# Optimization experiments

Hardware: AMD Instinct MI355X
Metric: run time of the kernel (lower is better)

## Reference

```python
import jax, jax.numpy as jnp
import numpy as np

NUM_GRAPHS = 2048


def gcn_conv(x, W, b, edge, N):
    # PyG GCNConv: x' = D^{-1/2} (A + I) D^{-1/2} (x W) + b
    src, dst = edge[0], edge[1]
    loop = jnp.arange(N, dtype=src.dtype)
    src = jnp.concatenate([src, loop])
    dst = jnp.concatenate([dst, loop])
    h = x @ W  # [N, out]
    deg = jax.ops.segment_sum(jnp.ones(dst.shape, x.dtype), dst, num_segments=N)
    dinv = jnp.where(deg > 0, jax.lax.rsqrt(deg), 0.0)
    norm = dinv[src] * dinv[dst]  # [E+N]
    out = jax.ops.segment_sum(h[src] * norm[:, None], dst, num_segments=N)
    return out + b


def pool_max_mean(x, batch, G):
    mx = jax.ops.segment_max(x, batch, num_segments=G)
    mx = jnp.where(jnp.isfinite(mx), mx, 0.0)  # guard empty segments
    s = jax.ops.segment_sum(x, batch, num_segments=G)
    cnt = jax.ops.segment_sum(jnp.ones((x.shape[0],), x.dtype), batch, num_segments=G)
    mean = s / jnp.maximum(cnt, 1.0)[:, None]
    return mx, mean


def setup_inputs() -> dict:
    key = jax.random.key(0)
    ks = jax.random.split(key, 20)
    F, CE, SE, DD = 64, 64, 32, 128
    Nc, Ec, Ns, Es = 100000, 1250000, 100000, 1250000

    def glorot(k, shape):
        fan_in, fan_out = shape[0], shape[1]
        lim = np.sqrt(6.0 / (fan_in + fan_out)).astype(np.float32)
        return jax.random.uniform(k, shape, jnp.float32, -lim, lim)

    inp = {
        "c": jax.random.normal(ks[0], (Nc, F), jnp.float32),
        "c_edge": jax.random.randint(ks[1], (2, Ec), 0, Nc),
        "c_batch": jnp.sort(jax.random.randint(ks[2], (Nc,), 0, NUM_GRAPHS)),
        "s": jax.random.normal(ks[3], (Ns, F), jnp.float32),
        "s_edge": jax.random.randint(ks[4], (2, Es), 0, Ns),
        "s_batch": jnp.sort(jax.random.randint(ks[5], (Ns,), 0, NUM_GRAPHS)),
        "Wc0": glorot(ks[6], (F, CE)), "bc0": jnp.zeros((CE,), jnp.float32),
        "Wc1": glorot(ks[7], (CE, CE)), "bc1": jnp.zeros((CE,), jnp.float32),
        "Wc2": glorot(ks[8], (CE, CE)), "bc2": jnp.zeros((CE,), jnp.float32),
        "Ws0": glorot(ks[9], (F, SE)), "bs0": jnp.zeros((SE,), jnp.float32),
        "Ws1": glorot(ks[10], (SE, SE)), "bs1": jnp.zeros((SE,), jnp.float32),
        "Ws2": glorot(ks[11], (SE, SE)), "bs2": jnp.zeros((SE,), jnp.float32),
        "Wd": glorot(ks[12], ((CE + SE) * 2, DD)), "bd": jnp.zeros((DD,), jnp.float32),
        "Wo": glorot(ks[13], (DD, 1)), "bo": jnp.zeros((1,), jnp.float32),
    }
    return inp


def reference(c, c_edge, c_batch, s, s_edge, s_batch,
              Wc0, bc0, Wc1, bc1, Wc2, bc2,
              Ws0, bs0, Ws1, bs1, Ws2, bs2,
              Wd, bd, Wo, bo):
    Nc, Ns = c.shape[0], s.shape[0]
    cro = jax.nn.relu(gcn_conv(c, Wc0, bc0, c_edge, Nc))
    cro = jax.nn.relu(gcn_conv(cro, Wc1, bc1, c_edge, Nc))
    cro = jax.nn.relu(gcn_conv(cro, Wc2, bc2, c_edge, Nc))
    solv = jax.nn.relu(gcn_conv(s, Ws0, bs0, s_edge, Ns))
    solv = jax.nn.relu(gcn_conv(solv, Ws1, bs1, s_edge, Ns))
    solv = jax.nn.relu(gcn_conv(solv, Ws2, bs2, s_edge, Ns))
    c_mx, c_mean = pool_max_mean(cro, c_batch, NUM_GRAPHS)
    s_mx, s_mean = pool_max_mean(solv, s_batch, NUM_GRAPHS)
    embed = jnp.concatenate([c_mx, c_mean, s_mx, s_mean], axis=1)  # [G, 192]
    dense = jax.nn.relu(embed @ Wd + bd)
    out = dense @ Wo + bo  # [G, 1]
    return out, embed
```

## Files before the change

kernel.cpp:

```cpp
#include <hip/hip_runtime.h>
#include <hip/hip_fp16.h>
#include <math.h>


static inline int cdiv(int a, int b) { return (a + b - 1) / b; }

#define BUCKET_CAP 8192
#define P1_CHUNK   4096

typedef _Float16 v8h __attribute__((ext_vector_type(8)));
typedef float    v4f __attribute__((ext_vector_type(4)));

__global__ void zero_int(int* __restrict__ p, int n) {
    int i = blockIdx.x * blockDim.x + threadIdx.x;
    if (i < n) p[i] = 0;
}

__global__ __launch_bounds__(256) void p1_partition(const int* __restrict__ c_edge, int Ec,
                                                    const int* __restrict__ s_edge, int Es,
                                                    int Nc_pad, int Etot, int nbuck,
                                                    int* __restrict__ bucket_fill,
                                                    unsigned* __restrict__ pk) {
    __shared__ unsigned       wbuf[P1_CHUNK];
    __shared__ unsigned short bbuf[P1_CHUNK];
    __shared__ int            hist[512];
    int e0 = blockIdx.x * P1_CHUNK;
    int n  = Etot - e0;
    if (n > P1_CHUNK) n = P1_CHUNK;
    for (int i = threadIdx.x; i < nbuck; i += 256) hist[i] = 0;
    __syncthreads();
    for (int i = threadIdx.x; i < n; i += 256) {
        int e = e0 + i, src, g;
        if (e < Ec) { src = c_edge[e]; g = c_edge[Ec + e]; }
        else        { int e2 = e - Ec; src = s_edge[e2]; g = Nc_pad + s_edge[Es + e2]; }
        int b   = g >> 9;
        wbuf[i] = ((unsigned)(g & 511) << 17) | (unsigned)src;
        bbuf[i] = (unsigned short)b;
        atomicAdd(&hist[b], 1);
    }
    __syncthreads();
    for (int i = threadIdx.x; i < nbuck; i += 256) {
        int h = hist[i];
        hist[i] = h ? atomicAdd(&bucket_fill[i], h) : 0;
    }
    __syncthreads();
    for (int i = threadIdx.x; i < n; i += 256) {
        int b    = bbuf[i];
        int slot = atomicAdd(&hist[b], 1);
        if (slot < BUCKET_CAP) pk[(size_t)b * BUCKET_CAP + slot] = wbuf[i];
    }
}

__global__ __launch_bounds__(512) void p2_scanbuckets(const int* __restrict__ fill, int nbuck,
                                                      int* __restrict__ basearr,
                                                      int* __restrict__ off_all, int Ntot_pad, int Etot) {
    __shared__ int sh[512];
    int v = (threadIdx.x < nbuck) ? fill[threadIdx.x] : 0;
    sh[threadIdx.x] = v;
    __syncthreads();
    for (int ofs = 1; ofs < 512; ofs <<= 1) {
        int t = (threadIdx.x >= ofs) ? sh[threadIdx.x - ofs] : 0;
        __syncthreads();
        sh[threadIdx.x] += t;
        __syncthreads();
    }
    if (threadIdx.x < nbuck) basearr[threadIdx.x] = sh[threadIdx.x] - v;
    if (threadIdx.x == 0) off_all[Ntot_pad] = Etot;
}

__global__ __launch_bounds__(512) void p3_build(const unsigned* __restrict__ pk,
                                                const int* __restrict__ fillarr,
                                                const int* __restrict__ basearr,
                                                int* __restrict__ off_all,
                                                float* __restrict__ dinv,
                                                int* __restrict__ csr) {
    __shared__ int sh[512];
    int b    = blockIdx.x;
    int fill = fillarr[b];
    if (fill > BUCKET_CAP) fill = BUCKET_CAP;
    int base = basearr[b];
    const unsigned* reg = pk + (size_t)b * BUCKET_CAP;
    sh[threadIdx.x] = 0;
    __syncthreads();
    for (int i = threadIdx.x; i < fill; i += 512) atomicAdd(&sh[reg[i] >> 17], 1);
    __syncthreads();
    int cnt = sh[threadIdx.x];
    for (int ofs = 1; ofs < 512; ofs <<= 1) {
        int t = (threadIdx.x >= ofs) ? sh[threadIdx.x - ofs] : 0;
        __syncthreads();
        sh[threadIdx.x] += t;
        __syncthreads();
    }
    int excl = sh[threadIdx.x] - cnt;
    int node = b * 512 + threadIdx.x;
    off_all[node] = base + excl;
    dinv[node]    = rsqrtf((float)(cnt + 1));
    __syncthreads();
    sh[threadIdx.x] = excl;
    __syncthreads();
    for (int i = threadIdx.x; i < fill; i += 512) {
        unsigned w    = reg[i];
        int      slot = atomicAdd(&sh[w >> 17], 1);
        csr[base + slot] = (int)(w & 0x1FFFFu);
    }
}

template <int K, int M, typename TIN>
__device__ void gemm_mfma(int bid, const TIN* __restrict__ X, const float* __restrict__ W,
                          const float* __restrict__ dinv, __half* __restrict__ H, int N,
                          char* smem_) {
    constexpr int RB = 64;
    constexpr int KP = K + 8;
    constexpr int NT = M / 16;
    constexpr int KS = K / 32;
    _Float16* Xh = (_Float16*)smem_;
    _Float16* Wz = Xh + RB * KP;
    const int t    = threadIdx.x;
    const int row0 = bid * RB;

    constexpr int WENT = NT * KS * 64;
    for (int idx = t; idx < WENT; idx += 256) {
        int lane = idx & 63, rest = idx >> 6;
        int ks = rest % KS, ntl = rest / KS;
        int kbase = ks * 32 + (lane >> 4) * 8;
        int col   = ntl * 16 + (lane & 15);
        union { float4 f4; _Float16 h[8]; } u;
#pragma unroll
        for (int j = 0; j < 8; ++j) u.h[j] = (_Float16)W[(kbase + j) * M + col];
        *(float4*)(Wz + idx * 8) = u.f4;
    }
    if constexpr (sizeof(TIN) == 4) {
        constexpr int NI = RB * K / 4;
        for (int idx = t; idx < NI; idx += 256) {
            int row = idx / (K / 4), k4 = idx % (K / 4);
            int gr = row0 + row;
            float4 v = make_float4(0.f, 0.f, 0.f, 0.f);
            if (gr < N) v = *(const float4*)((const float*)X + (size_t)gr * K + k4 * 4);
            union { float2 f2; _Float16 h[4]; } u;
            u.h[0] = (_Float16)v.x; u.h[1] = (_Float16)v.y;
            u.h[2] = (_Float16)v.z; u.h[3] = (_Float16)v.w;
            *(float2*)(Xh + row * KP + k4 * 4) = u.f2;
        }
    } else {
        constexpr int NI = RB * K / 8;
        for (int idx = t; idx < NI; idx += 256) {
            int row = idx / (K / 8), k8 = idx % (K / 8);
            int gr = row0 + row;
            float4 v = make_float4(0.f, 0.f, 0.f, 0.f);
            if (gr < N) v = *(const float4*)((const __half*)X + (size_t)gr * K + k8 * 8);
            *(float4*)(Xh + row * KP + k8 * 8) = v;
        }
    }
    __syncthreads();

    const int wave = t >> 6, lane = t & 63;
    const int quad = lane >> 4, nl = lane & 15;
    const int rowA = wave * 16 + nl;

    v4f acc[NT];
#pragma unroll
    for (int i = 0; i < NT; ++i) acc[i] = (v4f){0.f, 0.f, 0.f, 0.f};

#pragma unroll
    for (int ks = 0; ks < KS; ++ks) {
        v8h a = *(const v8h*)(Xh + rowA * KP + ks * 32 + quad * 8);
#pragma unroll
        for (int ntl = 0; ntl < NT; ++ntl) {
            v8h b = *(const v8h*)(Wz + ((ntl * KS + ks) * 64 + lane) * 8);
            acc[ntl] = __builtin_amdgcn_mfma_f32_16x16x32_f16(a, b, acc[ntl], 0, 0, 0);
        }
    }

#pragma unroll
    for (int r = 0; r < 4; ++r) {
        int gr = row0 + wave * 16 + quad * 4 + r;
        if (gr < N) {
            float dv = dinv[gr];
#pragma unroll
            for (int ntl = 0; ntl < NT; ++ntl)
                H[(size_t)gr * M + ntl * 16 + nl] = __float2half(acc[ntl][r] * dv);
        }
    }
}

__device__ __forceinline__ float4 load4h(const float2* __restrict__ base, size_t idx) {
    float2 r = base[idx];
    union { float2 f2; __half2 h2[2]; } u;
    u.f2 = r;
    float2 a = __half22float2(u.h2[0]);
    float2 b = __half22float2(u.h2[1]);
    return make_float4(a.x, a.y, b.x, b.y);
}

template <int M>
__device__ void agg_body(int bid, const __half* __restrict__ H,
                         const int* __restrict__ off_g,
                         const int* __restrict__ csr,
                         const float* __restrict__ dinv_g,
                         const float* __restrict__ b,
                         __half* __restrict__ out, int Nloc) {
    constexpr int L   = M / 4;
    constexpr int NPW = 64 / L;
    int lane = threadIdx.x & 63;
    int wave = threadIdx.x >> 6;
    int fq   = lane & (L - 1);
    int sub  = lane / L;
    int node = (bid * 4 + wave) * NPW + sub;
    if (node >= Nloc) return;
    const float2* H4 = (const float2*)H;
    int j0 = off_g[node], j1 = off_g[node + 1];
    float4 acc = load4h(H4, (size_t)node * L + fq);
    int j = j0;
    for (; j + 8 <= j1; j += 8) {
        int s0 = csr[j],     s1 = csr[j + 1], s2 = csr[j + 2], s3 = csr[j + 3];
        int s4 = csr[j + 4], s5 = csr[j + 5], s6 = csr[j + 6], s7 = csr[j + 7];
        float4 a0 = load4h(H4, (size_t)s0 * L + fq);
        float4 a1 = load4h(H4, (size_t)s1 * L + fq);
        float4 a2 = load4h(H4, (size_t)s2 * L + fq);
        float4 a3 = load4h(H4, (size_t)s3 * L + fq);
        float4 a4 = load4h(H4, (size_t)s4 * L + fq);
        float4 a5 = load4h(H4, (size_t)s5 * L + fq);
        float4 a6 = load4h(H4, (size_t)s6 * L + fq);
        float4 a7 = load4h(H4, (size_t)s7 * L + fq);
        acc.x += (a0.x + a1.x + a2.x + a3.x) + (a4.x + a5.x + a6.x + a7.x);
        acc.y += (a0.y + a1.y + a2.y + a3.y) + (a4.y + a5.y + a6.y + a7.y);
        acc.z += (a0.z + a1.z + a2.z + a3.z) + (a4.z + a5.z + a6.z + a7.z);
        acc.w += (a0.w + a1.w + a2.w + a3.w) + (a4.w + a5.w + a6.w + a7.w);
    }
    for (; j + 4 <= j1; j += 4) {
        int s0 = csr[j], s1 = csr[j + 1], s2 = csr[j + 2], s3 = csr[j + 3];
        float4 a0 = load4h(H4, (size_t)s0 * L + fq);
        float4 a1 = load4h(H4, (size_t)s1 * L + fq);
        float4 a2 = load4h(H4, (size_t)s2 * L + fq);
        float4 a3 = load4h(H4, (size_t)s3 * L + fq);
        acc.x += a0.x + a1.x + a2.x + a3.x;
        acc.y += a0.y + a1.y + a2.y + a3.y;
        acc.z += a0.z + a1.z + a2.z + a3.z;
        acc.w += a0.w + a1.w + a2.w + a3.w;
    }
    for (; j < j1; ++j) {
        float4 a = load4h(H4, (size_t)csr[j] * L + fq);
        acc.x += a.x; acc.y += a.y; acc.z += a.z; acc.w += a.w;
    }
    float  dv = dinv_g[node];
    float4 bb = ((const float4*)b)[fq];
    float  vx = dv * acc.x + bb.x;
    float  vy = dv * acc.y + bb.y;
    float  vz = dv * acc.z + bb.z;
    float  vw = dv * acc.w + bb.w;
    union { float2 f2; __half2 h2[2]; } o;
    o.h2[0] = __floats2half2_rn(vx > 0.f ? vx : 0.f, vy > 0.f ? vy : 0.f);
    o.h2[1] = __floats2half2_rn(vz > 0.f ? vz : 0.f, vw > 0.f ? vw : 0.f);
    ((float2*)out)[(size_t)node * L + fq] = o.f2;
}

__global__ __launch_bounds__(256) void gemmBoth0(const float* __restrict__ Xc, const float* __restrict__ Wc,
                                                 __half* __restrict__ cH, int Nc,
                                                 const float* __restrict__ Xs, const float* __restrict__ Ws,
                                                 __half* __restrict__ sH, int Ns,
                                                 const float* __restrict__ dinv_all, int Nc_pad, int nbC) {
    __shared__ __align__(16) char smem[17408];
    if (blockIdx.x < nbC) gemm_mfma<64, 64, float>(blockIdx.x, Xc, Wc, dinv_all, cH, Nc, smem);
    else                  gemm_mfma<64, 32, float>(blockIdx.x - nbC, Xs, Ws, dinv_all + Nc_pad, sH, Ns, smem);
}

__global__ __launch_bounds__(256) void gemmBoth(const __half* __restrict__ Xc, const float* __restrict__ Wc,
                                                __half* __restrict__ cH, int Nc,
                                                const __half* __restrict__ Xs, const float* __restrict__ Ws,
                                                __half* __restrict__ sH, int Ns,
                                                const float* __restrict__ dinv_all, int Nc_pad, int nbC) {
    __shared__ __align__(16) char smem[17408];
    if (blockIdx.x < nbC) gemm_mfma<64, 64, __half>(blockIdx.x, Xc, Wc, dinv_all, cH, Nc, smem);
    else                  gemm_mfma<32, 32, __half>(blockIdx.x - nbC, Xs, Ws, dinv_all + Nc_pad, sH, Ns, smem);
}

__global__ __launch_bounds__(256) void aggBoth(const __half* __restrict__ cH, const __half* __restrict__ sH,
                                               const int* __restrict__ off_all, const int* __restrict__ csr_all,
                                               const float* __restrict__ dinv_all,
                                               const float* __restrict__ bc, const float* __restrict__ bs,
                                               __half* __restrict__ outc, __half* __restrict__ outs,
                                               int Nc, int Ns, int Nc_pad, int nbC) {
    if (blockIdx.x < nbC)
        agg_body<64>(blockIdx.x, cH, off_all, csr_all, dinv_all, bc, outc, Nc);
    else
        agg_body<32>(blockIdx.x - nbC, sH, off_all + Nc_pad, csr_all,
                     dinv_all + Nc_pad, bs, outs, Ns);
}

__device__ __forceinline__ int lbound(const int* __restrict__ a, int n, int key) {
    int lo = 0, hi = n;
    while (lo < hi) {
        int mid = (lo + hi) >> 1;
        if (a[mid] < key) lo = mid + 1; else hi = mid;
    }
    return lo;
}

__global__ __launch_bounds__(128) void poolDense(const __half* __restrict__ cX, const int* __restrict__ c_batch, int Nc,
                                                 const __half* __restrict__ sX, const int* __restrict__ s_batch, int Ns,
                                                 const float* __restrict__ Wd, const float* __restrict__ bd,
                                                 const float* __restrict__ Wo, const float* __restrict__ bo,
                                                 float* __restrict__ outv, float* __restrict__ embed) {
    __shared__ float e[192];
    __shared__ float red[128];
    int g = blockIdx.x, t = threadIdx.x;
    if (t < 64) {
        int lo = lbound(c_batch, Nc, g), hi = lbound(c_batch, Nc, g + 1);
        float mx = 0.f, sm = 0.f;
        for (int i = lo; i < hi; ++i) {
            float v = __half2float(cX[(size_t)i * 64 + t]);
            mx = fmaxf(mx, v); sm += v;
        }
        int cn = hi - lo;
        e[t]      = mx;
        e[64 + t] = sm / (float)(cn > 0 ? cn : 1);
    } else if (t < 96) {
        int f  = t - 64;
        int lo = lbound(s_batch, Ns, g), hi = lbound(s_batch, Ns, g + 1);
        float mx = 0.f, sm = 0.f;
        for (int i = lo; i < hi; ++i) {
            float v = __half2float(sX[(size_t)i * 32 + f]);
            mx = fmaxf(mx, v); sm += v;
        }
        int cn = hi - lo;
        e[128 + f] = mx;
        e[160 + f] = sm / (float)(cn > 0 ? cn : 1);
    }
    __syncthreads();
    for (int k = t; k < 192; k += 128) embed[(size_t)g * 192 + k] = e[k];
    float acc = bd[t];
    for (int k = 0; k < 192; ++k) acc += e[k] * Wd[k * 128 + t];
    float d = acc > 0.f ? acc : 0.f;
    red[t]  = d * Wo[t];
    __syncthreads();
    for (int ofs = 64; ofs > 0; ofs >>= 1) {
        if (t < ofs) red[t] += red[t + ofs];
        __syncthreads();
    }
    if (t == 0) outv[g] = red[0] + bo[0];
}


extern "C" void kernel_launch(void* const* d_in, const int* in_sizes, int n_in,
                              void* d_out, int out_size, void* d_ws, size_t ws_size,
                              hipStream_t stream) {
    const float* c       = (const float*)d_in[0];
    const int*   c_edge  = (const int*)d_in[1];
    const int*   c_batch = (const int*)d_in[2];
    const float* s       = (const float*)d_in[3];
    const int*   s_edge  = (const int*)d_in[4];
    const int*   s_batch = (const int*)d_in[5];
    const float* Wc0 = (const float*)d_in[6],  *bc0 = (const float*)d_in[7];
    const float* Wc1 = (const float*)d_in[8],  *bc1 = (const float*)d_in[9];
    const float* Wc2 = (const float*)d_in[10], *bc2 = (const float*)d_in[11];
    const float* Ws0 = (const float*)d_in[12], *bs0 = (const float*)d_in[13];
    const float* Ws1 = (const float*)d_in[14], *bs1 = (const float*)d_in[15];
    const float* Ws2 = (const float*)d_in[16], *bs2 = (const float*)d_in[17];
    const float* Wd  = (const float*)d_in[18], *bd  = (const float*)d_in[19];
    const float* Wo  = (const float*)d_in[20], *bo  = (const float*)d_in[21];

    const int Nc = in_sizes[0] / 64;
    const int Ec = in_sizes[1] / 2;
    const int Ns = in_sizes[3] / 64;
    const int Es = in_sizes[4] / 2;
    const int G  = out_size / 193;
    const int Nc_pad   = cdiv(Nc, 512) * 512;
    const int Ns_pad   = cdiv(Ns, 512) * 512;
    const int Ntot_pad = Nc_pad + Ns_pad;
    const int Etot     = Ec + Es;
    const int nbuck    = Ntot_pad >> 9;

    char* p = (char*)d_ws;
    auto  alloc = [&](size_t bytes) -> void* {
        void* r = (void*)p;
        p += (bytes + 255) & ~(size_t)255;
        return r;
    };
    int*      bucket_fill = (int*)alloc(512 * 4);
    int*      bucket_base = (int*)alloc(512 * 4);
    unsigned* pk          = (unsigned*)alloc((size_t)nbuck * BUCKET_CAP * 4);
    int*      off_all     = (int*)alloc(((size_t)Ntot_pad + 1) * 4);
    int*      csr_all     = (int*)alloc((size_t)Etot * 4);
    float*    dinv_all    = (float*)alloc((size_t)Ntot_pad * 4);
    __half*   bufC        = (__half*)alloc((size_t)Nc * 64 * 2);
    __half*   bufS        = (__half*)alloc((size_t)Ns * 32 * 2);
    __half*   cH          = (__half*)alloc((size_t)Nc * 64 * 2);
    __half*   sH          = (__half*)alloc((size_t)Ns * 32 * 2);

    float* outv  = (float*)d_out;
    float* embed = outv + G;

    const int nbGmC = cdiv(Nc, 64), nbGmS = cdiv(Ns, 64);
    const int nbAgC = Nc_pad / 16,  nbAgS = Ns_pad / 32;

    zero_int<<<cdiv(nbuck, 256), 256, 0, stream>>>(bucket_fill, nbuck);
    p1_partition<<<cdiv(Etot, P1_CHUNK), 256, 0, stream>>>(c_edge, Ec, s_edge, Es,
                                                           Nc_pad, Etot, nbuck, bucket_fill, pk);
    p2_scanbuckets<<<1, 512, 0, stream>>>(bucket_fill, nbuck, bucket_base, off_all, Ntot_pad, Etot);
    p3_build<<<nbuck, 512, 0, stream>>>(pk, bucket_fill, bucket_base,
                                        off_all, dinv_all, csr_all);

    gemmBoth0<<<nbGmC + nbGmS, 256, 0, stream>>>(c, Wc0, cH, Nc, s, Ws0, sH, Ns,
                                                 dinv_all, Nc_pad, nbGmC);
    aggBoth<<<nbAgC + nbAgS, 256, 0, stream>>>(cH, sH, off_all, csr_all, dinv_all,
                                               bc0, bs0, bufC, bufS, Nc, Ns, Nc_pad, nbAgC);
    gemmBoth<<<nbGmC + nbGmS, 256, 0, stream>>>(bufC, Wc1, cH, Nc, bufS, Ws1, sH, Ns,
                                                dinv_all, Nc_pad, nbGmC);
    aggBoth<<<nbAgC + nbAgS, 256, 0, stream>>>(cH, sH, off_all, csr_all, dinv_all,
                                               bc1, bs1, bufC, bufS, Nc, Ns, Nc_pad, nbAgC);
    gemmBoth<<<nbGmC + nbGmS, 256, 0, stream>>>(bufC, Wc2, cH, Nc, bufS, Ws2, sH, Ns,
                                                dinv_all, Nc_pad, nbGmC);
    aggBoth<<<nbAgC + nbAgS, 256, 0, stream>>>(cH, sH, off_all, csr_all, dinv_all,
                                               bc2, bs2, bufC, bufS, Nc, Ns, Nc_pad, nbAgC);

    poolDense<<<G, 128, 0, stream>>>(bufC, c_batch, Nc, bufS, s_batch, Ns,
                                     Wd, bd, Wo, bo, outv, embed);
}
```

Before: 372.8 us.

## Stagger chem and solvent GCN stages so gemm and aggregation share launches

Offsets the solvent pipeline by half a stage so each launch pairs a compute-bound GEMM of one graph with the memory-bound aggregation of the other. Blocks of the two kinds are interleaved across the grid by a proportional split function. The chem pooling is folded into the last solvent aggregation launch. Both pooling loops now use four row groups per feature with a shared-memory reduction instead of one serial thread per feature. The launch count stays about the same, but blocks with different resource profiles share a kernel, so register and LDS usage follow the heavier path.

Result: no change. 376.4 us (+1.0%).

```diff
diff --git a/kernel.cpp b/kernel.cpp
--- a/kernel.cpp
+++ b/kernel.cpp
@@ -254,37 +254,50 @@
     ((float2*)out)[(size_t)node * L + fq] = o.f2;
 }
 
-__global__ __launch_bounds__(256) void gemmBoth0(const float* __restrict__ Xc, const float* __restrict__ Wc,
-                                                 __half* __restrict__ cH, int Nc,
-                                                 const float* __restrict__ Xs, const float* __restrict__ Ws,
-                                                 __half* __restrict__ sH, int Ns,
-                                                 const float* __restrict__ dinv_all, int Nc_pad, int nbC) {
+__device__ __forceinline__ bool split_grid(int bid, int nMaj, int nMin, int& idx) {
+    int T  = nMaj + nMin;
+    int g0 = (int)(((long long)bid * nMin) / T);
+    int g1 = (int)(((long long)(bid + 1) * nMin) / T);
+    if (g1 > g0) { idx = g0; return true; }
+    idx = bid - g0;
+    return false;
+}
+
+__global__ __launch_bounds__(256) void gemmC0(const float* __restrict__ Xc, const float* __restrict__ Wc,
+                                              __half* __restrict__ cH, int Nc,
+                                              const float* __restrict__ dinv_all) {
     __shared__ __align__(16) char smem[17408];
-    if (blockIdx.x < nbC) gemm_mfma<64, 64, float>(blockIdx.x, Xc, Wc, dinv_all, cH, Nc, smem);
-    else                  gemm_mfma<64, 32, float>(blockIdx.x - nbC, Xs, Ws, dinv_all + Nc_pad, sH, Ns, smem);
-}
-
-__global__ __launch_bounds__(256) void gemmBoth(const __half* __restrict__ Xc, const float* __restrict__ Wc,
-                                                __half* __restrict__ cH, int Nc,
-                                                const __half* __restrict__ Xs, const float* __restrict__ Ws,
-                                                __half* __restrict__ sH, int Ns,
-                                                const float* __restrict__ dinv_all, int Nc_pad, int nbC) {
+    gemm_mfma<64, 64, float>(blockIdx.x, Xc, Wc, dinv_all, cH, Nc, smem);
+}
+
+template <typename TIN, int K>
+__global__ __launch_bounds__(256) void aggC_gemmS(
+        const __half* __restrict__ cH, const int* __restrict__ off_c, const int* __restrict__ csr,
+        const float* __restrict__ dinv_all, const float* __restrict__ bc,
+        __half* __restrict__ outc, int Nc,
+        const TIN* __restrict__ Xs, const float* __restrict__ Ws, __half* __restrict__ sH, int Ns,
+        int Nc_pad, int nAgg, int nGem) {
     __shared__ __align__(16) char smem[17408];
-    if (blockIdx.x < nbC) gemm_mfma<64, 64, __half>(blockIdx.x, Xc, Wc, dinv_all, cH, Nc, smem);
-    else                  gemm_mfma<32, 32, __half>(blockIdx.x - nbC, Xs, Ws, dinv_all + Nc_pad, sH, Ns, smem);
-}
-
-__global__ __launch_bounds__(256) void aggBoth(const __half* __restrict__ cH, const __half* __restrict__ sH,
-                                               const int* __restrict__ off_all, const int* __restrict__ csr_all,
-                                               const float* __restrict__ dinv_all,
-                                               const float* __restrict__ bc, const float* __restrict__ bs,
-                                               __half* __restrict__ outc, __half* __restrict__ outs,
-                                               int Nc, int Ns, int Nc_pad, int nbC) {
-    if (blockIdx.x < nbC)
-        agg_body<64>(blockIdx.x, cH, off_all, csr_all, dinv_all, bc, outc, Nc);
+    int idx;
+    if (split_grid(blockIdx.x, nAgg, nGem, idx))
+        gemm_mfma<K, 32, TIN>(idx, Xs, Ws, dinv_all + Nc_pad, sH, Ns, smem);
     else
-        agg_body<32>(blockIdx.x - nbC, sH, off_all + Nc_pad, csr_all,
-                     dinv_all + Nc_pad, bs, outs, Ns);
+        agg_body<64>(idx, cH, off_c, csr, dinv_all, bc, outc, Nc);
+}
+
+__global__ __launch_bounds__(256) void gemmC_aggS(
+        const __half* __restrict__ Xc, const float* __restrict__ Wc,
+        __half* __restrict__ cH, int Nc,
+        const __half* __restrict__ sH, const int* __restrict__ off_all, const int* __restrict__ csr,
+        const float* __restrict__ dinv_all, const float* __restrict__ bs,
+        __half* __restrict__ outs, int Ns,
+        int Nc_pad, int nAgg, int nGem) {
+    __shared__ __align__(16) char smem[17408];
+    int idx;
+    if (split_grid(blockIdx.x, nAgg, nGem, idx))
+        gemm_mfma<64, 64, __half>(idx, Xc, Wc, dinv_all, cH, Nc, smem);
+    else
+        agg_body<32>(idx, sH, off_all + Nc_pad, csr, dinv_all + Nc_pad, bs, outs, Ns);
 }
 
 __device__ __forceinline__ int lbound(const int* __restrict__ a, int n, int key) {
@@ -296,38 +309,68 @@
     return lo;
 }
 
-__global__ __launch_bounds__(128) void poolDense(const __half* __restrict__ cX, const int* __restrict__ c_batch, int Nc,
-                                                 const __half* __restrict__ sX, const int* __restrict__ s_batch, int Ns,
-                                                 const float* __restrict__ Wd, const float* __restrict__ bd,
-                                                 const float* __restrict__ Wo, const float* __restrict__ bo,
-                                                 float* __restrict__ outv, float* __restrict__ embed) {
+__global__ __launch_bounds__(256) void aggS_poolC(
+        const __half* __restrict__ sH, const int* __restrict__ off_s, const int* __restrict__ csr,
+        const float* __restrict__ dinv_s, const float* __restrict__ bs,
+        __half* __restrict__ outs, int Ns,
+        const __half* __restrict__ cX, const int* __restrict__ c_batch, int Nc,
+        float* __restrict__ embed, int nAgg, int nPool) {
+    __shared__ float red[2][4][64];
+    int idx;
+    if (split_grid(blockIdx.x, nAgg, nPool, idx)) {
+        int g = idx, t = threadIdx.x;
+        int f = t & 63, grp = t >> 6;
+        int lo = lbound(c_batch, Nc, g), hi = lbound(c_batch, Nc, g + 1);
+        float mx = 0.f, sm = 0.f;
+        for (int i = lo + grp; i < hi; i += 4) {
+            float v = __half2float(cX[(size_t)i * 64 + f]);
+            mx = fmaxf(mx, v); sm += v;
+        }
+        red[0][grp][f] = mx; red[1][grp][f] = sm;
+        __syncthreads();
+        if (grp == 0) {
+            float m = fmaxf(fmaxf(red[0][0][f], red[0][1][f]),
+                            fmaxf(red[0][2][f], red[0][3][f]));
+            float s = (red[1][0][f] + red[1][1][f]) + (red[1][2][f] + red[1][3][f]);
+            int cn = hi - lo;
+            embed[(size_t)g * 192 + f]      = m;
+            embed[(size_t)g * 192 + 64 + f] = s / (float)(cn > 0 ? cn : 1);
+        }
+    } else {
+        agg_body<32>(idx, sH, off_s, csr, dinv_s, bs, outs, Ns);
+    }
+}
+
+__global__ __launch_bounds__(128) void poolS_dense(
+        const __half* __restrict__ sX, const int* __restrict__ s_batch, int Ns,
+        const float* __restrict__ Wd, const float* __restrict__ bd,
+        const float* __restrict__ Wo, const float* __restrict__ bo,
+        float* __restrict__ outv, float* __restrict__ embed) {
     __shared__ float e[192];
     __shared__ float red[128];
+    __shared__ float pr[2][4][32];
     int g = blockIdx.x, t = threadIdx.x;
-    if (t < 64) {
-        int lo = lbound(c_batch, Nc, g), hi = lbound(c_batch, Nc, g + 1);
-        float mx = 0.f, sm = 0.f;
-        for (int i = lo; i < hi; ++i) {
-            float v = __half2float(cX[(size_t)i * 64 + t]);
-            mx = fmaxf(mx, v); sm += v;
-        }
+    int f = t & 31, grp = t >> 5;
+    int lo = lbound(s_batch, Ns, g), hi = lbound(s_batch, Ns, g + 1);
+    float mx = 0.f, sm = 0.f;
+    for (int i = lo + grp; i < hi; i += 4) {
+        float v = __half2float(sX[(size_t)i * 32 + f]);
+        mx = fmaxf(mx, v); sm += v;
+    }
+    pr[0][grp][f] = mx; pr[1][grp][f] = sm;
+    e[t] = embed[(size_t)g * 192 + t];
+    __syncthreads();
+    if (t < 32) {
+        float m = fmaxf(fmaxf(pr[0][0][t], pr[0][1][t]), fmaxf(pr[0][2][t], pr[0][3][t]));
+        float s = (pr[1][0][t] + pr[1][1][t]) + (pr[1][2][t] + pr[1][3][t]);
         int cn = hi - lo;
-        e[t]      = mx;
-        e[64 + t] = sm / (float)(cn > 0 ? cn : 1);
-    } else if (t < 96) {
-        int f  = t - 64;
-        int lo = lbound(s_batch, Ns, g), hi = lbound(s_batch, Ns, g + 1);
-        float mx = 0.f, sm = 0.f;
-        for (int i = lo; i < hi; ++i) {
-            float v = __half2float(sX[(size_t)i * 32 + f]);
-            mx = fmaxf(mx, v); sm += v;
-        }
-        int cn = hi - lo;
-        e[128 + f] = mx;
-        e[160 + f] = sm / (float)(cn > 0 ? cn : 1);
-    }
-    __syncthreads();
-    for (int k = t; k < 192; k += 128) embed[(size_t)g * 192 + k] = e[k];
+        float mean = s / (float)(cn > 0 ? cn : 1);
+        e[128 + t] = m;
+        e[160 + t] = mean;
+        embed[(size_t)g * 192 + 128 + t] = m;
+        embed[(size_t)g * 192 + 160 + t] = mean;
+    }
+    __syncthreads();
     float acc = bd[t];
     for (int k = 0; k < 192; ++k) acc += e[k] * Wd[k * 128 + t];
     float d = acc > 0.f ? acc : 0.f;
@@ -400,19 +443,27 @@
     p3_build<<<nbuck, 512, 0, stream>>>(pk, bucket_fill, bucket_base,
                                         off_all, dinv_all, csr_all);
 
-    gemmBoth0<<<nbGmC + nbGmS, 256, 0, stream>>>(c, Wc0, cH, Nc, s, Ws0, sH, Ns,
-                                                 dinv_all, Nc_pad, nbGmC);
-    aggBoth<<<nbAgC + nbAgS, 256, 0, stream>>>(cH, sH, off_all, csr_all, dinv_all,
-                                               bc0, bs0, bufC, bufS, Nc, Ns, Nc_pad, nbAgC);
-    gemmBoth<<<nbGmC + nbGmS, 256, 0, stream>>>(bufC, Wc1, cH, Nc, bufS, Ws1, sH, Ns,
-                                                dinv_all, Nc_pad, nbGmC);
-    aggBoth<<<nbAgC + nbAgS, 256, 0, stream>>>(cH, sH, off_all, csr_all, dinv_all,
-                                               bc1, bs1, bufC, bufS, Nc, Ns, Nc_pad, nbAgC);
-    gemmBoth<<<nbGmC + nbGmS, 256, 0, stream>>>(bufC, Wc2, cH, Nc, bufS, Ws2, sH, Ns,
-                                                dinv_all, Nc_pad, nbGmC);
-    aggBoth<<<nbAgC + nbAgS, 256, 0, stream>>>(cH, sH, off_all, csr_all, dinv_all,
-                                               bc2, bs2, bufC, bufS, Nc, Ns, Nc_pad, nbAgC);
-
-    poolDense<<<G, 128, 0, stream>>>(bufC, c_batch, Nc, bufS, s_batch, Ns,
-                                     Wd, bd, Wo, bo, outv, embed);
-}
+    gemmC0<<<nbGmC, 256, 0, stream>>>(c, Wc0, cH, Nc, dinv_all);
+
+    aggC_gemmS<float, 64><<<nbAgC + nbGmS, 256, 0, stream>>>(
+        cH, off_all, csr_all, dinv_all, bc0, bufC, Nc,
+        s, Ws0, sH, Ns, Nc_pad, nbAgC, nbGmS);
+    gemmC_aggS<<<nbGmC + nbAgS, 256, 0, stream>>>(
+        bufC, Wc1, cH, Nc,
+        sH, off_all, csr_all, dinv_all, bs0, bufS, Ns, Nc_pad, nbAgS, nbGmC);
+    aggC_gemmS<__half, 32><<<nbAgC + nbGmS, 256, 0, stream>>>(
+        cH, off_all, csr_all, dinv_all, bc1, bufC, Nc,
+        bufS, Ws1, sH, Ns, Nc_pad, nbAgC, nbGmS);
+    gemmC_aggS<<<nbGmC + nbAgS, 256, 0, stream>>>(
+        bufC, Wc2, cH, Nc,
+        sH, off_all, csr_all, dinv_all, bs1, bufS, Ns, Nc_pad, nbAgS, nbGmC);
+    aggC_gemmS<__half, 32><<<nbAgC + nbGmS, 256, 0, stream>>>(
+        cH, off_all, csr_all, dinv_all, bc2, bufC, Nc,
+        bufS, Ws2, sH, Ns, Nc_pad, nbAgC, nbGmS);
+
+    aggS_poolC<<<nbAgS + G, 256, 0, stream>>>(
+        sH, off_all + Nc_pad, csr_all, dinv_all + Nc_pad, bs2, bufS, Ns,
+        bufC, c_batch, Nc, embed, nbAgS, G);
+
+    poolS_dense<<<G, 128, 0, stream>>>(bufS, s_batch, Ns, Wd, bd, Wo, bo, outv, embed);
+}
```

## Fuse GCN aggregation with next layer's MFMA GEMM and parallelize pooling

Applied to the files above, without the earlier changes.

Adds a fused kernel in which each block aggregates 64 nodes' neighbour features (8 halves per lane, gathers unrolled by 8) into shared memory, applies bias and ReLU, then runs the next layer's weight multiply with MFMA and writes the pre-scaled output. This removes the round trip of the intermediate activations through global memory and two kernel launches. Ping-pong buffers are used because the fused kernel reads neighbour rows while writing new ones. Separately, poolDense grows to 256 threads and splits each graph's node range across several thread groups with a shared-memory reduction, instead of one thread per feature walking every node. The cost is that each fused block also has to convert and stage the weight matrix, and it holds more shared memory and registers.

New measurement: 355.5 us. -4.6%, faster.

```diff
diff --git a/kernel.cpp b/kernel.cpp
--- a/kernel.cpp
+++ b/kernel.cpp
@@ -190,6 +190,143 @@
     float2 a = __half22float2(u.h2[0]);
     float2 b = __half22float2(u.h2[1]);
     return make_float4(a.x, a.y, b.x, b.y);
+}
+
+__device__ __forceinline__ void load8h(const float4* __restrict__ base, size_t idx,
+                                       float* __restrict__ o) {
+    float4 r = base[idx];
+    union { float4 f4; __half2 h2[4]; } u;
+    u.f4 = r;
+    float2 p0 = __half22float2(u.h2[0]);
+    float2 p1 = __half22float2(u.h2[1]);
+    float2 p2 = __half22float2(u.h2[2]);
+    float2 p3 = __half22float2(u.h2[3]);
+    o[0] = p0.x; o[1] = p0.y; o[2] = p1.x; o[3] = p1.y;
+    o[4] = p2.x; o[5] = p2.y; o[6] = p3.x; o[7] = p3.y;
+}
+
+template <int MF>
+__device__ void fused_agg_gemm(int bid, const __half* __restrict__ Hin,
+                               const int* __restrict__ off_g, const int* __restrict__ csr,
+                               const float* __restrict__ dinv_g, const float* __restrict__ b,
+                               const float* __restrict__ W, __half* __restrict__ Hout,
+                               int N, char* smem_) {
+    constexpr int KP = MF + 8;
+    constexpr int NT = MF / 16;
+    constexpr int KS = MF / 32;
+    _Float16* Xh = (_Float16*)smem_;
+    _Float16* Wz = Xh + 64 * KP;
+    const int t = threadIdx.x;
+
+    constexpr int WENT = NT * KS * 64;
+    for (int idx = t; idx < WENT; idx += 256) {
+        int lane = idx & 63, rest = idx >> 6;
+        int ks = rest % KS, ntl = rest / KS;
+        int kbase = ks * 32 + (lane >> 4) * 8;
+        int col   = ntl * 16 + (lane & 15);
+        union { float4 f4; _Float16 h[8]; } u;
+#pragma unroll
+        for (int j = 0; j < 8; ++j) u.h[j] = (_Float16)W[(kbase + j) * MF + col];
+        *(float4*)(Wz + idx * 8) = u.f4;
+    }
+
+    constexpr int L      = MF / 8;
+    constexpr int NPW    = 64 / L;
+    constexpr int PASSES = 64 / (4 * NPW);
+    const int lane = t & 63, wave = t >> 6;
+    const int fq = lane & (L - 1), sub = lane / L;
+    const float4* H4 = (const float4*)Hin;
+    const float4* b4 = (const float4*)b;
+    float bb[8];
+    {
+        float4 b0 = b4[fq * 2], b1 = b4[fq * 2 + 1];
+        bb[0] = b0.x; bb[1] = b0.y; bb[2] = b0.z; bb[3] = b0.w;
+        bb[4] = b1.x; bb[5] = b1.y; bb[6] = b1.z; bb[7] = b1.w;
+    }
+#pragma unroll
+    for (int pass = 0; pass < PASSES; ++pass) {
+        int ln   = (pass * 4 + wave) * NPW + sub;
+        int node = bid * 64 + ln;
+        if (node < N) {
+            int j0 = off_g[node], j1 = off_g[node + 1];
+            float acc[8];
+            load8h(H4, (size_t)node * L + fq, acc);
+            int j = j0;
+            for (; j + 8 <= j1; j += 8) {
+                int s0 = csr[j],     s1 = csr[j + 1], s2 = csr[j + 2], s3 = csr[j + 3];
+                int s4 = csr[j + 4], s5 = csr[j + 5], s6 = csr[j + 6], s7 = csr[j + 7];
+                float a0[8], a1[8], a2[8], a3[8], a4[8], a5[8], a6[8], a7[8];
+                load8h(H4, (size_t)s0 * L + fq, a0);
+                load8h(H4, (size_t)s1 * L + fq, a1);
+                load8h(H4, (size_t)s2 * L + fq, a2);
+                load8h(H4, (size_t)s3 * L + fq, a3);
+                load8h(H4, (size_t)s4 * L + fq, a4);
+                load8h(H4, (size_t)s5 * L + fq, a5);
+                load8h(H4, (size_t)s6 * L + fq, a6);
+                load8h(H4, (size_t)s7 * L + fq, a7);
+#pragma unroll
+                for (int f = 0; f < 8; ++f) {
+                    float g1 = ((a0[f] + a1[f]) + a2[f]) + a3[f];
+                    float g2 = ((a4[f] + a5[f]) + a6[f]) + a7[f];
+                    acc[f] += g1 + g2;
+                }
+            }
+            for (; j + 4 <= j1; j += 4) {
+                int s0 = csr[j], s1 = csr[j + 1], s2 = csr[j + 2], s3 = csr[j + 3];
+                float a0[8], a1[8], a2[8], a3[8];
+                load8h(H4, (size_t)s0 * L + fq, a0);
+                load8h(H4, (size_t)s1 * L + fq, a1);
+                load8h(H4, (size_t)s2 * L + fq, a2);
+                load8h(H4, (size_t)s3 * L + fq, a3);
+#pragma unroll
+                for (int f = 0; f < 8; ++f)
+                    acc[f] += ((a0[f] + a1[f]) + a2[f]) + a3[f];
+            }
+            for (; j < j1; ++j) {
+                float a0[8];
+                load8h(H4, (size_t)csr[j] * L + fq, a0);
+#pragma unroll
+                for (int f = 0; f < 8; ++f) acc[f] += a0[f];
+            }
+            float dv = dinv_g[node];
+            union { float4 f4; __half2 h2[4]; } o;
+#pragma unroll
+            for (int p2 = 0; p2 < 4; ++p2) {
+                float vx = dv * acc[2 * p2]     + bb[2 * p2];
+                float vy = dv * acc[2 * p2 + 1] + bb[2 * p2 + 1];
+                o.h2[p2] = __floats2half2_rn(vx > 0.f ? vx : 0.f, vy > 0.f ? vy : 0.f);
+            }
+            *(float4*)(Xh + ln * KP + fq * 8) = o.f4;
+        } else {
+            *(float4*)(Xh + ln * KP + fq * 8) = make_float4(0.f, 0.f, 0.f, 0.f);
+        }
+    }
+    __syncthreads();
+
+    const int quad = lane >> 4, nl = lane & 15;
+    const int rowA = wave * 16 + nl;
+    v4f acc2[NT];
+#pragma unroll
+    for (int i = 0; i < NT; ++i) acc2[i] = (v4f){0.f, 0.f, 0.f, 0.f};
+#pragma unroll
+    for (int ks = 0; ks < KS; ++ks) {
+        v8h av = *(const v8h*)(Xh + rowA * KP + ks * 32 + quad * 8);
+#pragma unroll
+        for (int ntl = 0; ntl < NT; ++ntl) {
+            v8h bv = *(const v8h*)(Wz + ((ntl * KS + ks) * 64 + lane) * 8);
+            acc2[ntl] = __builtin_amdgcn_mfma_f32_16x16x32_f16(av, bv, acc2[ntl], 0, 0, 0);
+        }
+    }
+#pragma unroll
+    for (int r = 0; r < 4; ++r) {
+        int gr = bid * 64 + wave * 16 + quad * 4 + r;
+        if (gr < N) {
+            float dv = dinv_g[gr];
+#pragma unroll
+            for (int ntl = 0; ntl < NT; ++ntl)
+                Hout[(size_t)gr * MF + ntl * 16 + nl] = __float2half(acc2[ntl][r] * dv);
+        }
+    }
 }
 
 template <int M>
@@ -264,14 +401,20 @@
     else                  gemm_mfma<64, 32, float>(blockIdx.x - nbC, Xs, Ws, dinv_all + Nc_pad, sH, Ns, smem);
 }
 
-__global__ __launch_bounds__(256) void gemmBoth(const __half* __restrict__ Xc, const float* __restrict__ Wc,
-                                                __half* __restrict__ cH, int Nc,
-                                                const __half* __restrict__ Xs, const float* __restrict__ Ws,
-                                                __half* __restrict__ sH, int Ns,
-                                                const float* __restrict__ dinv_all, int Nc_pad, int nbC) {
+__global__ __launch_bounds__(256) void fusedBoth(
+        const __half* __restrict__ cHin, __half* __restrict__ cHout,
+        const float* __restrict__ Wc, const float* __restrict__ bc,
+        const __half* __restrict__ sHin, __half* __restrict__ sHout,
+        const float* __restrict__ Ws, const float* __restrict__ bs,
+        const int* __restrict__ off_all, const int* __restrict__ csr_all,
+        const float* __restrict__ dinv_all,
+        int Nc, int Ns, int Nc_pad, int nbC) {
     __shared__ __align__(16) char smem[17408];
-    if (blockIdx.x < nbC) gemm_mfma<64, 64, __half>(blockIdx.x, Xc, Wc, dinv_all, cH, Nc, smem);
-    else                  gemm_mfma<32, 32, __half>(blockIdx.x - nbC, Xs, Ws, dinv_all + Nc_pad, sH, Ns, smem);
+    if (blockIdx.x < nbC)
+        fused_agg_gemm<64>(blockIdx.x, cHin, off_all, csr_all, dinv_all, bc, Wc, cHout, Nc, smem);
+    else
+        fused_agg_gemm<32>(blockIdx.x - nbC, sHin, off_all + Nc_pad, csr_all,
+                           dinv_all + Nc_pad, bs, Ws, sHout, Ns, smem);
 }
 
 __global__ __launch_bounds__(256) void aggBoth(const __half* __restrict__ cH, const __half* __restrict__ sH,
@@ -296,48 +439,73 @@
     return lo;
 }
 
-__global__ __launch_bounds__(128) void poolDense(const __half* __restrict__ cX, const int* __restrict__ c_batch, int Nc,
+__global__ __launch_bounds__(256) void poolDense(const __half* __restrict__ cX, const int* __restrict__ c_batch, int Nc,
                                                  const __half* __restrict__ sX, const int* __restrict__ s_batch, int Ns,
                                                  const float* __restrict__ Wd, const float* __restrict__ bd,
                                                  const float* __restrict__ Wo, const float* __restrict__ bo,
                                                  float* __restrict__ outv, float* __restrict__ embed) {
     __shared__ float e[192];
-    __shared__ float red[128];
+    __shared__ float red[512];
+    __shared__ float rs[128];
     int g = blockIdx.x, t = threadIdx.x;
+    int clo = lbound(c_batch, Nc, g), chi = lbound(c_batch, Nc, g + 1);
+    {
+        int f = t & 63, grp = t >> 6;
+        float mx = 0.f, sm = 0.f;
+        for (int i = clo + grp; i < chi; i += 4) {
+            float v = __half2float(cX[(size_t)i * 64 + f]);
+            mx = fmaxf(mx, v); sm += v;
+        }
+        red[grp * 64 + f]       = mx;
+        red[256 + grp * 64 + f] = sm;
+    }
+    __syncthreads();
     if (t < 64) {
-        int lo = lbound(c_batch, Nc, g), hi = lbound(c_batch, Nc, g + 1);
+        float m = fmaxf(fmaxf(red[t], red[64 + t]), fmaxf(red[128 + t], red[192 + t]));
+        float s = (red[256 + t] + red[320 + t]) + (red[384 + t] + red[448 + t]);
+        int cn = chi - clo;
+        e[t]      = m;
+        e[64 + t] = s / (float)(cn > 0 ? cn : 1);
+    }
+    __syncthreads();
+    int slo = lbound(s_batch, Ns, g), shi = lbound(s_batch, Ns, g + 1);
+    {
+        int f = t & 31, grp = t >> 5;
         float mx = 0.f, sm = 0.f;
-        for (int i = lo; i < hi; ++i) {
-            float v = __half2float(cX[(size_t)i * 64 + t]);
-            mx = fmaxf(mx, v); sm += v;
-        }
-        int cn = hi - lo;
-        e[t]      = mx;
-        e[64 + t] = sm / (float)(cn > 0 ? cn : 1);
-    } else if (t < 96) {
-        int f  = t - 64;
-        int lo = lbound(s_batch, Ns, g), hi = lbound(s_batch, Ns, g + 1);
-        float mx = 0.f, sm = 0.f;
-        for (int i = lo; i < hi; ++i) {
+        for (int i = slo + grp; i < shi; i += 8) {
             float v = __half2float(sX[(size_t)i * 32 + f]);
             mx = fmaxf(mx, v); sm += v;
         }
-        int cn = hi - lo;
-        e[128 + f] = mx;
-        e[160 + f] = sm / (float)(cn > 0 ? cn : 1);
-    }
-    __syncthreads();
-    for (int k = t; k < 192; k += 128) embed[(size_t)g * 192 + k] = e[k];
-    float acc = bd[t];
-    for (int k = 0; k < 192; ++k) acc += e[k] * Wd[k * 128 + t];
-    float d = acc > 0.f ? acc : 0.f;
-    red[t]  = d * Wo[t];
+        red[grp * 32 + f]       = mx;
+        red[256 + grp * 32 + f] = sm;
+    }
+    __syncthreads();
+    if (t < 32) {
+        float m = red[t];
+        float s = red[256 + t];
+#pragma unroll
+        for (int grp = 1; grp < 8; ++grp) {
+            m  = fmaxf(m, red[grp * 32 + t]);
+            s += red[256 + grp * 32 + t];
+        }
+        int cn = shi - slo;
+        e[128 + t] = m;
+        e[160 + t] = s / (float)(cn > 0 ? cn : 1);
+    }
+    __syncthreads();
+    if (t < 192) embed[(size_t)g * 192 + t] = e[t];
+    if (t < 128) {
+        float acc = bd[t];
+        for (int k = 0; k < 192; ++k) acc += e[k] * Wd[k * 128 + t];
+        float d = acc > 0.f ? acc : 0.f;
+        rs[t] = d * Wo[t];
+    }
     __syncthreads();
     for (int ofs = 64; ofs > 0; ofs >>= 1) {
-        if (t < ofs) red[t] += red[t + ofs];
+        if (t < ofs) rs[t] += rs[t + ofs];
         __syncthreads();
     }
-    if (t == 0) outv[g] = red[0] + bo[0];
+    if (t == 0) outv[g] = rs[0] + bo[0];
 }
 
 
@@ -384,13 +552,16 @@
     float*    dinv_all    = (float*)alloc((size_t)Ntot_pad * 4);
     __half*   bufC        = (__half*)alloc((size_t)Nc * 64 * 2);
     __half*   bufS        = (__half*)alloc((size_t)Ns * 32 * 2);
-    __half*   cH          = (__half*)alloc((size_t)Nc * 64 * 2);
-    __half*   sH          = (__half*)alloc((size_t)Ns * 32 * 2);
+    __half*   cHa         = (__half*)alloc((size_t)Nc * 64 * 2);
+    __half*   cHb         = (__half*)alloc((size_t)Nc * 64 * 2);
+    __half*   sHa         = (__half*)alloc((size_t)Ns * 32 * 2);
+    __half*   sHb         = (__half*)alloc((size_t)Ns * 32 * 2);
 
     float* outv  = (float*)d_out;
     float* embed = outv + G;
 
     const int nbGmC = cdiv(Nc, 64), nbGmS = cdiv(Ns, 64);
+    const int nbFC  = cdiv(Nc, 64), nbFS  = cdiv(Ns, 64);
     const int nbAgC = Nc_pad / 16,  nbAgS = Ns_pad / 32;
 
     zero_int<<<cdiv(nbuck, 256), 256, 0, stream>>>(bucket_fill, nbuck);
@@ -400,19 +571,19 @@
     p3_build<<<nbuck, 512, 0, stream>>>(pk, bucket_fill, bucket_base,
                                         off_all, dinv_all, csr_all);
 
-    gemmBoth0<<<nbGmC + nbGmS, 256, 0, stream>>>(c, Wc0, cH, Nc, s, Ws0, sH, Ns,
+    gemmBoth0<<<nbGmC + nbGmS, 256, 0, stream>>>(c, Wc0, cHa, Nc, s, Ws0, sHa, Ns,
                                                  dinv_all, Nc_pad, nbGmC);
-    aggBoth<<<nbAgC + nbAgS, 256, 0, stream>>>(cH, sH, off_all, csr_all, dinv_all,
-                                               bc0, bs0, bufC, bufS, Nc, Ns, Nc_pad, nbAgC);
-    gemmBoth<<<nbGmC + nbGmS, 256, 0, stream>>>(bufC, Wc1, cH, Nc, bufS, Ws1, sH, Ns,
-                                                dinv_all, Nc_pad, nbGmC);
-    aggBoth<<<nbAgC + nbAgS, 256, 0, stream>>>(cH, sH, off_all, csr_all, dinv_all,
-                                               bc1, bs1, bufC, bufS, Nc, Ns, Nc_pad, nbAgC);
-    gemmBoth<<<nbGmC + nbGmS, 256, 0, stream>>>(bufC, Wc2, cH, Nc, bufS, Ws2, sH, Ns,
-                                                dinv_all, Nc_pad, nbGmC);
-    aggBoth<<<nbAgC + nbAgS, 256, 0, stream>>>(cH, sH, off_all, csr_all, dinv_all,
+
+    fusedBoth<<<nbFC + nbFS, 256, 0, stream>>>(cHa, cHb, Wc1, bc0, sHa, sHb, Ws1, bs0,
+                                               off_all, csr_all, dinv_all,
+                                               Nc, Ns, Nc_pad, nbFC);
+    fusedBoth<<<nbFC + nbFS, 256, 0, stream>>>(cHb, cHa, Wc2, bc1, sHb, sHa, Ws2, bs1,
+                                               off_all, csr_all, dinv_all,
+                                               Nc, Ns, Nc_pad, nbFC);
+
+    aggBoth<<<nbAgC + nbAgS, 256, 0, stream>>>(cHa, sHa, off_all, csr_all, dinv_all,
                                                bc2, bs2, bufC, bufS, Nc, Ns, Nc_pad, nbAgC);
 
-    poolDense<<<G, 128, 0, stream>>>(bufC, c_batch, Nc, bufS, s_batch, Ns,
+    poolDense<<<G, 256, 0, stream>>>(bufC, c_batch, Nc, bufS, s_batch, Ns,
                                      Wd, bd, Wo, bo, outv, embed);
 }
```
